# Performance work log

Measured on AMD Instinct MI355X. Metric: run time of the kernel, lower is better.

## Reference

```python
import jax, jax.numpy as jnp
import numpy as np

B, T, TOKEN_DIM, TPR_DIM = 16, 256, 256, 10
INNER = TOKEN_DIM // 4  # 64
TH = 32                 # tpr_mlp hidden dim
EPS = 1e-5              # BatchNorm eps


def _bn(x, g, b, m, v):
    # BatchNorm1d in eval mode: normalize with running stats
    return (x - m) * jax.lax.rsqrt(v + EPS) * g + b


def setup_inputs() -> dict:
    key = jax.random.key(0)
    ks = iter(jax.random.split(key, 32))
    def n(shape, s=0.02):
        return jax.random.normal(next(ks), shape, dtype=jnp.float32) * s
    def bn_params(c):
        g = 1.0 + 0.1 * jax.random.normal(next(ks), (c,), dtype=jnp.float32)
        b = 0.1 * jax.random.normal(next(ks), (c,), dtype=jnp.float32)
        m = 0.1 * jax.random.normal(next(ks), (c,), dtype=jnp.float32)
        v = jax.random.uniform(next(ks), (c,), dtype=jnp.float32, minval=0.5, maxval=1.5)
        return g, b, m, v
    inp = {}
    inp['x'] = jax.random.normal(next(ks), (B, T, TOKEN_DIM), dtype=jnp.float32)
    inp['r'] = jax.random.normal(next(ks), (B, T, T, TPR_DIM), dtype=jnp.float32)
    # fc1: Linear(token,token) + BN(token)
    inp['W1'] = n((TOKEN_DIM, TOKEN_DIM)); inp['b1'] = n((TOKEN_DIM,))
    inp['bn1_g'], inp['bn1_b'], inp['bn1_m'], inp['bn1_v'] = bn_params(TOKEN_DIM)
    # VectorAttention
    inp['Wqkv'] = n((TOKEN_DIM, 3 * INNER))
    inp['Wt1'] = n((TPR_DIM, TH)); inp['bt1'] = n((TH,))
    inp['bnt_g'], inp['bnt_b'], inp['bnt_m'], inp['bnt_v'] = bn_params(TH)
    inp['Wt2'] = n((TH, INNER)); inp['bt2'] = n((INNER,))
    inp['Wa1'] = n((INNER, INNER)); inp['ba1'] = n((INNER,))
    inp['Wa2'] = n((INNER, INNER)); inp['ba2'] = n((INNER,))
    # fc2: Linear(inner, token) + BN(token)
    inp['W2'] = n((INNER, TOKEN_DIM)); inp['b2'] = n((TOKEN_DIM,))
    inp['bn2_g'], inp['bn2_b'], inp['bn2_m'], inp['bn2_v'] = bn_params(TOKEN_DIM)
    return inp


def reference(x, r, W1, b1, bn1_g, bn1_b, bn1_m, bn1_v, Wqkv,
              Wt1, bt1, bnt_g, bnt_b, bnt_m, bnt_v, Wt2, bt2,
              Wa1, ba1, Wa2, ba2, W2, b2, bn2_g, bn2_b, bn2_m, bn2_v):
    # fc1 + BN, residual skip (pre-relu)
    y = _bn(x @ W1 + b1, bn1_g, bn1_b, bn1_m, bn1_v)  # [B,T,C]
    skip = y
    y = jax.nn.relu(y)
    # VectorAttention
    qkv = y @ Wqkv                                     # [B,T,3*inner]
    q, k, v = jnp.split(qkv, 3, axis=-1)               # each [B,T,inner]
    qk_rel = q[:, :, None, :] - k[:, None, :, :]       # [B,T,T,inner]
    rel_emb = jax.nn.relu(_bn(r @ Wt1 + bt1, bnt_g, bnt_b, bnt_m, bnt_v)) @ Wt2 + bt2  # [B,T,T,inner]
    vv = v[:, None, :, :] + rel_emb                    # [B,T,T,inner]
    h = jax.nn.relu((qk_rel + rel_emb) @ Wa1 + ba1)
    sim = h @ Wa2 + ba2                                # [B,T,T,inner]
    attn = jax.nn.softmax(sim, axis=-2)                # softmax over j (neighbor) axis
    agg = jnp.sum(attn * vv, axis=2)                   # [B,T,inner]
    # fc2 + BN + residual + relu
    out = jax.nn.relu(_bn(agg @ W2 + b2, bn2_g, bn2_b, bn2_m, bn2_v) + skip)
    return out  # [B,T,token_dim]
```

## Files before the change

kernel.cpp:

```cpp
#include <hip/hip_runtime.h>
#include <math.h>

#define BB 16
#define TT 256
#define CC 256
#define INNER 64
#define TPR 10
#define THD 32
#define EPSV 1e-5f

typedef __attribute__((ext_vector_type(8))) short short8;
typedef __attribute__((ext_vector_type(4))) float f32x4;

__device__ __forceinline__ short f2bf(float f) {
    unsigned u = __float_as_uint(f);
    u += 0x7fffu + ((u >> 16) & 1);
    return (short)(u >> 16);
}

__global__ __launch_bounds__(256) void fc1_qkv_kernel(
    const float* __restrict__ x, const float* __restrict__ W1, const float* __restrict__ b1,
    const float* __restrict__ g1, const float* __restrict__ bb1,
    const float* __restrict__ m1, const float* __restrict__ v1,
    const float* __restrict__ Wqkv,
    float* __restrict__ skip, float* __restrict__ qkv)
{
    const int ROWS = 8;
    __shared__ float xr[ROWS][CC];
    __shared__ float yr[ROWS][CC];
    const int n0 = blockIdx.x * ROWS;
    const int t = threadIdx.x;

#pragma unroll
    for (int rr = 0; rr < ROWS; ++rr)
        xr[rr][t] = x[(size_t)(n0 + rr) * CC + t];
    __syncthreads();

    float acc[ROWS];
#pragma unroll
    for (int rr = 0; rr < ROWS; ++rr) acc[rr] = 0.f;
    for (int k = 0; k < CC; ++k) {
        float wv = W1[(size_t)k * CC + t];
#pragma unroll
        for (int rr = 0; rr < ROWS; ++rr) acc[rr] = fmaf(xr[rr][k], wv, acc[rr]);
    }
    const float s1 = g1[t] * rsqrtf(v1[t] + EPSV);
    const float base = b1[t] - m1[t];
    const float bet = bb1[t];
#pragma unroll
    for (int rr = 0; rr < ROWS; ++rr) {
        float y = (acc[rr] + base) * s1 + bet;
        skip[(size_t)(n0 + rr) * CC + t] = y;
        yr[rr][t] = fmaxf(y, 0.f);
    }
    __syncthreads();

    if (t < 192) {
        float a2[ROWS];
#pragma unroll
        for (int rr = 0; rr < ROWS; ++rr) a2[rr] = 0.f;
        for (int k = 0; k < CC; ++k) {
            float wv = Wqkv[(size_t)k * 192 + t];
#pragma unroll
            for (int rr = 0; rr < ROWS; ++rr) a2[rr] = fmaf(yr[rr][k], wv, a2[rr]);
        }
#pragma unroll
        for (int rr = 0; rr < ROWS; ++rr)
            qkv[(size_t)(n0 + rr) * 192 + t] = a2[rr];
    }
}

#define O_TH   0
#define O_HID  32768
#define O_WA1  49152
#define O_WA2  57344
#define O_WT2  65536
#define O_WT1  69632
#define O_RED  71680
#define LDSZ   75776

__device__ __forceinline__ short8 ldfragA(const char* lds, int base, int row, int kbyte, int sl2, int mask) {
    return *(const short8*)(lds + base + (row << sl2) + (kbyte ^ ((row & mask) << 4)));
}
__device__ __forceinline__ void stbf16(char* lds, int base, int row, int col, int sl2, int mask, float v) {
    int cb = col * 2;
    int off = base + (row << sl2) + ((((cb & ~15) ^ ((row & mask) << 4))) | (cb & 15));
    *(short*)(lds + off) = f2bf(v);
}

__global__ __launch_bounds__(512) void attn_mfma_kernel(
    const float* __restrict__ r, const float* __restrict__ qkv,
    const float* __restrict__ Wt1, const float* __restrict__ bt1,
    const float* __restrict__ gt, const float* __restrict__ bbt,
    const float* __restrict__ mt, const float* __restrict__ vt,
    const float* __restrict__ Wt2, const float* __restrict__ bt2,
    const float* __restrict__ Wa1, const float* __restrict__ ba1,
    const float* __restrict__ Wa2, const float* __restrict__ ba2,
    float* __restrict__ agg)
{
    __shared__ char lds[LDSZ];
    const int n = blockIdx.x, b = n >> 8;
    const int tid = threadIdx.x;
    const int wv = tid >> 6, lane = tid & 63;
    const int lid = lane & 15, q4 = lane >> 4;
    const int kb = q4 * 16;
    const int tm0 = wv * 2;

    {
        uint32_t* z = (uint32_t*)lds;
#pragma unroll
        for (int e = 0; e < 8; ++e) z[tid + e * 512] = 0;
        ((uint32_t*)(lds + O_WT1))[tid] = 0;
    }
    __syncthreads();

    {
        const float* rrow = r + (size_t)n * (TT * TPR);
        for (int e = tid; e < TT * TPR; e += 512) {
            int j = e / TPR, p = e - j * TPR;
            int cb = p * 2;
            int off = (j << 6) + (((cb & ~15) ^ ((j & 3) << 4)) | (cb & 15));
            *(short*)(lds + off) = f2bf(rrow[e]);
        }
        if (tid < TPR * THD) {
            int p = tid >> 5, h = tid & 31;
            float scv = gt[h] * rsqrtf(vt[h] + EPSV);
            int cb = p * 2;
            int off = O_WT1 + (h << 6) + (((cb & ~15) ^ ((h & 3) << 4)) | (cb & 15));
            *(short*)(lds + off) = f2bf(Wt1[tid] * scv);
        }
        for (int e = tid; e < THD * INNER; e += 512) {
            int k = e >> 6, c = e & 63;
            int cb = k * 2;
            int off = O_WT2 + (c << 6) + (((cb & ~15) ^ ((c & 3) << 4)) | (cb & 15));
            *(short*)(lds + off) = f2bf(Wt2[e]);
        }
        for (int e = tid; e < INNER * INNER; e += 512) {
            int k = e >> 6, c = e & 63;
            int cb = k * 2;
            int sw = ((cb & ~15) ^ ((c & 7) << 4)) | (cb & 15);
            *(short*)(lds + O_WA1 + (c << 7) + sw) = f2bf(Wa1[e]);
            *(short*)(lds + O_WA2 + (c << 7) + sw) = f2bf(Wa2[e]);
        }
    }
    __syncthreads();

    {
        short8 b1f[2];
#pragma unroll
        for (int tn = 0; tn < 2; ++tn) {
            int cr = tn * 16 + lid;
            b1f[tn] = ldfragA(lds, O_WT1, cr, kb, 6, 3);
        }
        f32x4 acc1[2][2];
#pragma unroll
        for (int tm = 0; tm < 2; ++tm) {
            int row = (tm0 + tm) * 16 + lid;
            short8 a = ldfragA(lds, 0, row, kb, 6, 3);
#pragma unroll
            for (int tn = 0; tn < 2; ++tn) {
                f32x4 z = {0.f, 0.f, 0.f, 0.f};
                acc1[tm][tn] = __builtin_amdgcn_mfma_f32_16x16x32_bf16(a, b1f[tn], z, 0, 0, 0);
            }
        }
#pragma unroll
        for (int tn = 0; tn < 2; ++tn) {
            int col = tn * 16 + lid;
            float scv = gt[col] * rsqrtf(vt[col] + EPSV);
            float c1v = (bt1[col] - mt[col]) * scv + bbt[col];
#pragma unroll
            for (int tm = 0; tm < 2; ++tm)
#pragma unroll
                for (int g = 0; g < 4; ++g) {
                    int rw = (tm0 + tm) * 16 + q4 * 4 + g;
                    stbf16(lds, O_HID, rw, col, 6, 3, fmaxf(acc1[tm][tn][g] + c1v, 0.f));
                }
        }
    }
    __syncthreads();

    f32x4 rel[2][4];
    {
        short8 b2f[4];
#pragma unroll
        for (int tn = 0; tn < 4; ++tn) {
            int cr = tn * 16 + lid;
            b2f[tn] = ldfragA(lds, O_WT2, cr, kb, 6, 3);
        }
#pragma unroll
        for (int tm = 0; tm < 2; ++tm) {
            int row = (tm0 + tm) * 16 + lid;
            short8 a = ldfragA(lds, O_HID, row, kb, 6, 3);
#pragma unroll
            for (int tn = 0; tn < 4; ++tn) {
                f32x4 z = {0.f, 0.f, 0.f, 0.f};
                rel[tm][tn] = __builtin_amdgcn_mfma_f32_16x16x32_bf16(a, b2f[tn], z, 0, 0, 0);
            }
        }
    }
    const float* kvb = qkv + (size_t)b * (TT * 192);
#pragma unroll
    for (int tn = 0; tn < 4; ++tn) {
        int col = tn * 16 + lid;
        float bt2c = bt2[col];
        float qc = qkv[(size_t)n * 192 + col];
#pragma unroll
        for (int tm = 0; tm < 2; ++tm)
#pragma unroll
            for (int g = 0; g < 4; ++g) {
                int j = (tm0 + tm) * 16 + q4 * 4 + g;
                rel[tm][tn][g] += bt2c;
                float tv = qc - kvb[j * 192 + 64 + col] + rel[tm][tn][g];
                stbf16(lds, O_TH, j, col, 7, 7, tv);
            }
    }

    f32x4 acc[2][4];
#pragma unroll
    for (int tm = 0; tm < 2; ++tm)
#pragma unroll
        for (int tn = 0; tn < 4; ++tn) { f32x4 z = {0.f,0.f,0.f,0.f}; acc[tm][tn] = z; }
#pragma unroll
    for (int ks = 0; ks < 2; ++ks) {
        short8 bf[4];
#pragma unroll
        for (int tn = 0; tn < 4; ++tn) {
            int cr = tn * 16 + lid;
            bf[tn] = ldfragA(lds, O_WA1, cr, ks * 64 + kb, 7, 7);
        }
#pragma unroll
        for (int tm = 0; tm < 2; ++tm) {
            int row = (tm0 + tm) * 16 + lid;
            short8 a = ldfragA(lds, O_TH, row, ks * 64 + kb, 7, 7);
#pragma unroll
            for (int tn = 0; tn < 4; ++tn)
                acc[tm][tn] = __builtin_amdgcn_mfma_f32_16x16x32_bf16(a, bf[tn], acc[tm][tn], 0, 0, 0);
        }
    }
#pragma unroll
    for (int tn = 0; tn < 4; ++tn) {
        int col = tn * 16 + lid;
        float ba1c = ba1[col];
#pragma unroll
        for (int tm = 0; tm < 2; ++tm)
#pragma unroll
            for (int g = 0; g < 4; ++g) {
                int rw = (tm0 + tm) * 16 + q4 * 4 + g;
                stbf16(lds, O_TH, rw, col, 7, 7, fmaxf(acc[tm][tn][g] + ba1c, 0.f));
            }
    }

#pragma unroll
    for (int tm = 0; tm < 2; ++tm)
#pragma unroll
        for (int tn = 0; tn < 4; ++tn) { f32x4 z = {0.f,0.f,0.f,0.f}; acc[tm][tn] = z; }
#pragma unroll
    for (int ks = 0; ks < 2; ++ks) {
        short8 bf[4];
#pragma unroll
        for (int tn = 0; tn < 4; ++tn) {
            int cr = tn * 16 + lid;
            bf[tn] = ldfragA(lds, O_WA2, cr, ks * 64 + kb, 7, 7);
        }
#pragma unroll
        for (int tm = 0; tm < 2; ++tm) {
            int row = (tm0 + tm) * 16 + lid;
            short8 a = ldfragA(lds, O_TH, row, ks * 64 + kb, 7, 7);
#pragma unroll
            for (int tn = 0; tn < 4; ++tn)
                acc[tm][tn] = __builtin_amdgcn_mfma_f32_16x16x32_bf16(a, bf[tn], acc[tm][tn], 0, 0, 0);
        }
    }

    float num[4], den[4];
#pragma unroll
    for (int tn = 0; tn < 4; ++tn) { num[tn] = 0.f; den[tn] = 0.f; }
#pragma unroll
    for (int tn = 0; tn < 4; ++tn) {
        int col = tn * 16 + lid;
#pragma unroll
        for (int tm = 0; tm < 2; ++tm)
#pragma unroll
            for (int g = 0; g < 4; ++g) {
                int j = (tm0 + tm) * 16 + q4 * 4 + g;
                float ev = __expf(acc[tm][tn][g]);
                float vvv = kvb[j * 192 + 128 + col] + rel[tm][tn][g];
                den[tn] += ev;
                num[tn] = fmaf(ev, vvv, num[tn]);
            }
    }
#pragma unroll
    for (int tn = 0; tn < 4; ++tn) {
        num[tn] += __shfl_xor(num[tn], 16);
        num[tn] += __shfl_xor(num[tn], 32);
        den[tn] += __shfl_xor(den[tn], 16);
        den[tn] += __shfl_xor(den[tn], 32);
    }
    if (lane < 16) {
        float* RD = (float*)(lds + O_RED);
#pragma unroll
        for (int tn = 0; tn < 4; ++tn) {
            RD[(wv * 2 + 0) * 64 + tn * 16 + lane] = num[tn];
            RD[(wv * 2 + 1) * 64 + tn * 16 + lane] = den[tn];
        }
    }
    __syncthreads();
    if (tid < 64) {
        float* RD = (float*)(lds + O_RED);
        float nn = 0.f, dd = 0.f;
#pragma unroll
        for (int w = 0; w < 8; ++w) {
            nn += RD[(w * 2 + 0) * 64 + tid];
            dd += RD[(w * 2 + 1) * 64 + tid];
        }
        agg[(size_t)n * 64 + tid] = nn / dd;
    }
}

__global__ __launch_bounds__(256) void fc2_kernel(
    const float* __restrict__ agg, const float* __restrict__ W2, const float* __restrict__ b2,
    const float* __restrict__ g2, const float* __restrict__ bb2,
    const float* __restrict__ m2, const float* __restrict__ v2,
    const float* __restrict__ skip, float* __restrict__ out)
{
    const int ROWS = 8;
    __shared__ float ar[ROWS][INNER];
    const int n0 = blockIdx.x * ROWS;
    const int t = threadIdx.x;

    for (int idx = t; idx < ROWS * INNER; idx += 256)
        ((float*)ar)[idx] = agg[(size_t)n0 * INNER + idx];
    __syncthreads();

    const float s2 = g2[t] * rsqrtf(v2[t] + EPSV);
    const float base = b2[t] - m2[t];
    const float bet = bb2[t];

    float accv[ROWS];
#pragma unroll
    for (int rr = 0; rr < ROWS; ++rr) accv[rr] = 0.f;
    for (int k = 0; k < INNER; ++k) {
        float wv = W2[(size_t)k * CC + t];
#pragma unroll
        for (int rr = 0; rr < ROWS; ++rr) accv[rr] = fmaf(ar[rr][k], wv, accv[rr]);
    }
#pragma unroll
    for (int rr = 0; rr < ROWS; ++rr) {
        float y = (accv[rr] + base) * s2 + bet;
        out[(size_t)(n0 + rr) * CC + t] =
            fmaxf(y + skip[(size_t)(n0 + rr) * CC + t], 0.f);
    }
}

extern "C" void kernel_launch(void* const* d_in, const int* in_sizes, int n_in,
                              void* d_out, int out_size, void* d_ws, size_t ws_size,
                              hipStream_t stream)
{
    const float* x   = (const float*)d_in[0];
    const float* r   = (const float*)d_in[1];
    const float* W1  = (const float*)d_in[2];
    const float* b1  = (const float*)d_in[3];
    const float* g1  = (const float*)d_in[4];
    const float* bb1 = (const float*)d_in[5];
    const float* m1  = (const float*)d_in[6];
    const float* v1  = (const float*)d_in[7];
    const float* Wqkv= (const float*)d_in[8];
    const float* Wt1 = (const float*)d_in[9];
    const float* bt1 = (const float*)d_in[10];
    const float* gt  = (const float*)d_in[11];
    const float* bbt = (const float*)d_in[12];
    const float* mt  = (const float*)d_in[13];
    const float* vt  = (const float*)d_in[14];
    const float* Wt2 = (const float*)d_in[15];
    const float* bt2 = (const float*)d_in[16];
    const float* Wa1 = (const float*)d_in[17];
    const float* ba1 = (const float*)d_in[18];
    const float* Wa2 = (const float*)d_in[19];
    const float* ba2 = (const float*)d_in[20];
    const float* W2  = (const float*)d_in[21];
    const float* b2  = (const float*)d_in[22];
    const float* g2  = (const float*)d_in[23];
    const float* bb2 = (const float*)d_in[24];
    const float* m2  = (const float*)d_in[25];
    const float* v2  = (const float*)d_in[26];
    float* out = (float*)d_out;

    const int N = BB * TT;
    float* skip = (float*)d_ws;
    float* qkv  = skip + (size_t)N * CC;
    float* agg  = qkv  + (size_t)N * 192;

    fc1_qkv_kernel<<<dim3(N / 8), dim3(256), 0, stream>>>(
        x, W1, b1, g1, bb1, m1, v1, Wqkv, skip, qkv);
    attn_mfma_kernel<<<dim3(N), dim3(512), 0, stream>>>(
        r, qkv, Wt1, bt1, gt, bbt, mt, vt, Wt2, bt2, Wa1, ba1, Wa2, ba2, agg);
    fc2_kernel<<<dim3(N / 8), dim3(256), 0, stream>>>(
        agg, W2, b2, g2, bb2, m2, v2, skip, out);
}
```

Baseline: 169.1 us.

## Transpose MFMA operands so each wave owns its j rows, dropping a barrier

The attention kernel now computes every matmul in transposed form, with weights as the A operand and neighbor rows as B. Each lane then holds four consecutive channels for one j, so global loads of k, v and BN params become float4 vector loads and LDS stores become packed 8-byte bf16 writes. Because each wave only reads and writes its own j rows of the shared activation tile, the __syncthreads between the tpr MLP stages goes away. The final reduction changes to shuffles over the j lanes, and launch bounds request 4 waves per SIMD at a slightly larger LDS footprint, which may raise register pressure.

```diff
diff --git a/kernel.cpp b/kernel.cpp
--- a/kernel.cpp
+++ b/kernel.cpp
@@ -1,4 +1,5 @@
 #include <hip/hip_runtime.h>
+#include <hip/hip_bf16.h>
 #include <math.h>
 
 #define BB 16
@@ -11,11 +12,15 @@
 
 typedef __attribute__((ext_vector_type(8))) short short8;
 typedef __attribute__((ext_vector_type(4))) float f32x4;
+typedef __attribute__((ext_vector_type(4))) unsigned int u32x4;
 
 __device__ __forceinline__ short f2bf(float f) {
     unsigned u = __float_as_uint(f);
     u += 0x7fffu + ((u >> 16) & 1);
     return (short)(u >> 16);
+}
+__device__ __forceinline__ unsigned pkbf(float a, float b) {
+    return (unsigned)(unsigned short)f2bf(a) | ((unsigned)(unsigned short)f2bf(b) << 16);
 }
 
 __global__ __launch_bounds__(256) void fc1_qkv_kernel(
@@ -70,25 +75,23 @@
     }
 }
 
-#define O_TH   0
-#define O_HID  32768
-#define O_WA1  49152
-#define O_WA2  57344
-#define O_WT2  65536
-#define O_WT1  69632
-#define O_RED  71680
-#define LDSZ   75776
-
-__device__ __forceinline__ short8 ldfragA(const char* lds, int base, int row, int kbyte, int sl2, int mask) {
-    return *(const short8*)(lds + base + (row << sl2) + (kbyte ^ ((row & mask) << 4)));
-}
-__device__ __forceinline__ void stbf16(char* lds, int base, int row, int col, int sl2, int mask, float v) {
-    int cb = col * 2;
-    int off = base + (row << sl2) + ((((cb & ~15) ^ ((row & mask) << 4))) | (cb & 15));
-    *(short*)(lds + off) = f2bf(v);
-}
-
-__global__ __launch_bounds__(512) void attn_mfma_kernel(
+#define O_R    0
+#define O_TH   16384
+#define O_WT1  49152
+#define O_WT2  53248
+#define O_WA1  61440
+#define O_WA2  69632
+#define O_RED  77824
+#define LDSZ   81920
+
+__device__ __forceinline__ int swb(int row, int cb, int sh, int mask) {
+    return (row << sh) + (((cb & ~15) ^ ((row & mask) << 4)) | (cb & 15));
+}
+__device__ __forceinline__ short8 ldfrag(const char* lds, int base, int row, int cb16, int sh, int mask) {
+    return *(const short8*)(lds + base + (row << sh) + (cb16 ^ ((row & mask) << 4)));
+}
+
+__global__ __launch_bounds__(512, 4) void attn_mfma_kernel(
     const float* __restrict__ r, const float* __restrict__ qkv,
     const float* __restrict__ Wt1, const float* __restrict__ bt1,
     const float* __restrict__ gt, const float* __restrict__ bbt,
@@ -98,19 +101,19 @@
     const float* __restrict__ Wa2, const float* __restrict__ ba2,
     float* __restrict__ agg)
 {
-    __shared__ char lds[LDSZ];
+    __shared__ __align__(16) char lds[LDSZ];
     const int n = blockIdx.x, b = n >> 8;
     const int tid = threadIdx.x;
     const int wv = tid >> 6, lane = tid & 63;
     const int lid = lane & 15, q4 = lane >> 4;
     const int kb = q4 * 16;
-    const int tm0 = wv * 2;
+    const int jt0 = wv * 2;
 
     {
-        uint32_t* z = (uint32_t*)lds;
-#pragma unroll
-        for (int e = 0; e < 8; ++e) z[tid + e * 512] = 0;
-        ((uint32_t*)(lds + O_WT1))[tid] = 0;
+        u32x4 z = {0u, 0u, 0u, 0u};
+        *(u32x4*)(lds + O_R + tid * 16) = z;
+        *(u32x4*)(lds + O_R + 8192 + tid * 16) = z;
+        if (tid < 256) *(u32x4*)(lds + O_WT1 + tid * 16) = z;
     }
     __syncthreads();
 
@@ -118,200 +121,195 @@
         const float* rrow = r + (size_t)n * (TT * TPR);
         for (int e = tid; e < TT * TPR; e += 512) {
             int j = e / TPR, p = e - j * TPR;
-            int cb = p * 2;
-            int off = (j << 6) + (((cb & ~15) ^ ((j & 3) << 4)) | (cb & 15));
-            *(short*)(lds + off) = f2bf(rrow[e]);
+            *(short*)(lds + O_R + swb(j, p * 2, 6, 3)) = f2bf(rrow[e]);
         }
         if (tid < TPR * THD) {
             int p = tid >> 5, h = tid & 31;
             float scv = gt[h] * rsqrtf(vt[h] + EPSV);
-            int cb = p * 2;
-            int off = O_WT1 + (h << 6) + (((cb & ~15) ^ ((h & 3) << 4)) | (cb & 15));
-            *(short*)(lds + off) = f2bf(Wt1[tid] * scv);
+            *(short*)(lds + O_WT1 + swb(h, p * 2, 7, 7)) = f2bf(Wt1[tid] * scv);
         }
         for (int e = tid; e < THD * INNER; e += 512) {
-            int k = e >> 6, c = e & 63;
-            int cb = k * 2;
-            int off = O_WT2 + (c << 6) + (((cb & ~15) ^ ((c & 3) << 4)) | (cb & 15));
-            *(short*)(lds + off) = f2bf(Wt2[e]);
+            int h = e >> 6, c = e & 63;
+            *(short*)(lds + O_WT2 + swb(c, h * 2, 7, 7)) = f2bf(Wt2[e]);
         }
         for (int e = tid; e < INNER * INNER; e += 512) {
             int k = e >> 6, c = e & 63;
-            int cb = k * 2;
-            int sw = ((cb & ~15) ^ ((c & 7) << 4)) | (cb & 15);
-            *(short*)(lds + O_WA1 + (c << 7) + sw) = f2bf(Wa1[e]);
-            *(short*)(lds + O_WA2 + (c << 7) + sw) = f2bf(Wa2[e]);
-        }
-    }
-    __syncthreads();
+            *(short*)(lds + O_WA1 + swb(c, k * 2, 7, 7)) = f2bf(Wa1[e]);
+            *(short*)(lds + O_WA2 + swb(c, k * 2, 7, 7)) = f2bf(Wa2[e]);
+        }
+    }
+    __syncthreads();
+
+    const float* kvb = qkv + (size_t)b * (TT * 192);
+    const f32x4 z4 = {0.f, 0.f, 0.f, 0.f};
 
     {
-        short8 b1f[2];
-#pragma unroll
-        for (int tn = 0; tn < 2; ++tn) {
-            int cr = tn * 16 + lid;
-            b1f[tn] = ldfragA(lds, O_WT1, cr, kb, 6, 3);
-        }
+        short8 aw0 = ldfrag(lds, O_WT1, lid, kb, 7, 7);
+        short8 aw1 = ldfrag(lds, O_WT1, 16 + lid, kb, 7, 7);
         f32x4 acc1[2][2];
 #pragma unroll
+        for (int tn = 0; tn < 2; ++tn) {
+            int j = (jt0 + tn) * 16 + lid;
+            short8 bf = ldfrag(lds, O_R, j, kb, 6, 3);
+            acc1[0][tn] = __builtin_amdgcn_mfma_f32_16x16x32_bf16(aw0, bf, z4, 0, 0, 0);
+            acc1[1][tn] = __builtin_amdgcn_mfma_f32_16x16x32_bf16(aw1, bf, z4, 0, 0, 0);
+        }
+#pragma unroll
         for (int tm = 0; tm < 2; ++tm) {
-            int row = (tm0 + tm) * 16 + lid;
-            short8 a = ldfragA(lds, 0, row, kb, 6, 3);
+            int ch0 = tm * 16 + q4 * 4;
+            f32x4 g4 = *(const f32x4*)(gt + ch0);
+            f32x4 vv4 = *(const f32x4*)(vt + ch0);
+            f32x4 b4 = *(const f32x4*)(bt1 + ch0);
+            f32x4 m4 = *(const f32x4*)(mt + ch0);
+            f32x4 bb4 = *(const f32x4*)(bbt + ch0);
+            f32x4 c1;
+#pragma unroll
+            for (int g = 0; g < 4; ++g)
+                c1[g] = (b4[g] - m4[g]) * (g4[g] * rsqrtf(vv4[g] + EPSV)) + bb4[g];
 #pragma unroll
             for (int tn = 0; tn < 2; ++tn) {
-                f32x4 z = {0.f, 0.f, 0.f, 0.f};
-                acc1[tm][tn] = __builtin_amdgcn_mfma_f32_16x16x32_bf16(a, b1f[tn], z, 0, 0, 0);
+                int j = (jt0 + tn) * 16 + lid;
+                float h0 = fmaxf(acc1[tm][tn][0] + c1[0], 0.f);
+                float h1 = fmaxf(acc1[tm][tn][1] + c1[1], 0.f);
+                float h2 = fmaxf(acc1[tm][tn][2] + c1[2], 0.f);
+                float h3 = fmaxf(acc1[tm][tn][3] + c1[3], 0.f);
+                uint2 w; w.x = pkbf(h0, h1); w.y = pkbf(h2, h3);
+                *(uint2*)(lds + O_TH + swb(j, tm * 32 + q4 * 8, 7, 7)) = w;
             }
         }
-#pragma unroll
-        for (int tn = 0; tn < 2; ++tn) {
-            int col = tn * 16 + lid;
-            float scv = gt[col] * rsqrtf(vt[col] + EPSV);
-            float c1v = (bt1[col] - mt[col]) * scv + bbt[col];
-#pragma unroll
-            for (int tm = 0; tm < 2; ++tm)
-#pragma unroll
-                for (int g = 0; g < 4; ++g) {
-                    int rw = (tm0 + tm) * 16 + q4 * 4 + g;
-                    stbf16(lds, O_HID, rw, col, 6, 3, fmaxf(acc1[tm][tn][g] + c1v, 0.f));
-                }
-        }
-    }
-    __syncthreads();
-
-    f32x4 rel[2][4];
+    }
+
+    f32x4 rel[4][2];
     {
-        short8 b2f[4];
-#pragma unroll
-        for (int tn = 0; tn < 4; ++tn) {
-            int cr = tn * 16 + lid;
-            b2f[tn] = ldfragA(lds, O_WT2, cr, kb, 6, 3);
-        }
-#pragma unroll
-        for (int tm = 0; tm < 2; ++tm) {
-            int row = (tm0 + tm) * 16 + lid;
-            short8 a = ldfragA(lds, O_HID, row, kb, 6, 3);
-#pragma unroll
-            for (int tn = 0; tn < 4; ++tn) {
-                f32x4 z = {0.f, 0.f, 0.f, 0.f};
-                rel[tm][tn] = __builtin_amdgcn_mfma_f32_16x16x32_bf16(a, b2f[tn], z, 0, 0, 0);
+        short8 aw[4];
+#pragma unroll
+        for (int tm = 0; tm < 4; ++tm)
+            aw[tm] = ldfrag(lds, O_WT2, tm * 16 + lid, kb, 7, 7);
+#pragma unroll
+        for (int tn = 0; tn < 2; ++tn) {
+            int j = (jt0 + tn) * 16 + lid;
+            short8 bf = ldfrag(lds, O_TH, j, kb, 7, 7);
+#pragma unroll
+            for (int tm = 0; tm < 4; ++tm)
+                rel[tm][tn] = __builtin_amdgcn_mfma_f32_16x16x32_bf16(aw[tm], bf, z4, 0, 0, 0);
+        }
+    }
+#pragma unroll
+    for (int tm = 0; tm < 4; ++tm) {
+        int ch0 = tm * 16 + q4 * 4;
+        f32x4 bt24 = *(const f32x4*)(bt2 + ch0);
+        f32x4 qv4 = *(const f32x4*)(qkv + (size_t)n * 192 + ch0);
+#pragma unroll
+        for (int tn = 0; tn < 2; ++tn) {
+            int j = (jt0 + tn) * 16 + lid;
+            f32x4 kv4 = *(const f32x4*)(kvb + (size_t)j * 192 + 64 + ch0);
+            float t0, t1, t2, t3;
+#pragma unroll
+            for (int g = 0; g < 4; ++g) rel[tm][tn][g] += bt24[g];
+            t0 = qv4[0] - kv4[0] + rel[tm][tn][0];
+            t1 = qv4[1] - kv4[1] + rel[tm][tn][1];
+            t2 = qv4[2] - kv4[2] + rel[tm][tn][2];
+            t3 = qv4[3] - kv4[3] + rel[tm][tn][3];
+            uint2 w; w.x = pkbf(t0, t1); w.y = pkbf(t2, t3);
+            *(uint2*)(lds + O_TH + swb(j, tm * 32 + q4 * 8, 7, 7)) = w;
+        }
+    }
+
+    f32x4 acc[4][2];
+#pragma unroll
+    for (int tm = 0; tm < 4; ++tm)
+#pragma unroll
+        for (int tn = 0; tn < 2; ++tn) acc[tm][tn] = z4;
+#pragma unroll
+    for (int ks = 0; ks < 2; ++ks) {
+        short8 aw[4];
+#pragma unroll
+        for (int tm = 0; tm < 4; ++tm)
+            aw[tm] = ldfrag(lds, O_WA1, tm * 16 + lid, ks * 64 + kb, 7, 7);
+#pragma unroll
+        for (int tn = 0; tn < 2; ++tn) {
+            int j = (jt0 + tn) * 16 + lid;
+            short8 bf = ldfrag(lds, O_TH, j, ks * 64 + kb, 7, 7);
+#pragma unroll
+            for (int tm = 0; tm < 4; ++tm)
+                acc[tm][tn] = __builtin_amdgcn_mfma_f32_16x16x32_bf16(aw[tm], bf, acc[tm][tn], 0, 0, 0);
+        }
+    }
+#pragma unroll
+    for (int tm = 0; tm < 4; ++tm) {
+        int ch0 = tm * 16 + q4 * 4;
+        f32x4 ba14 = *(const f32x4*)(ba1 + ch0);
+#pragma unroll
+        for (int tn = 0; tn < 2; ++tn) {
+            int j = (jt0 + tn) * 16 + lid;
+            float h0 = fmaxf(acc[tm][tn][0] + ba14[0], 0.f);
+            float h1 = fmaxf(acc[tm][tn][1] + ba14[1], 0.f);
+            float h2 = fmaxf(acc[tm][tn][2] + ba14[2], 0.f);
+            float h3 = fmaxf(acc[tm][tn][3] + ba14[3], 0.f);
+            uint2 w; w.x = pkbf(h0, h1); w.y = pkbf(h2, h3);
+            *(uint2*)(lds + O_TH + swb(j, tm * 32 + q4 * 8, 7, 7)) = w;
+        }
+    }
+
+#pragma unroll
+    for (int tm = 0; tm < 4; ++tm)
+#pragma unroll
+        for (int tn = 0; tn < 2; ++tn) acc[tm][tn] = z4;
+#pragma unroll
+    for (int ks = 0; ks < 2; ++ks) {
+        short8 aw[4];
+#pragma unroll
+        for (int tm = 0; tm < 4; ++tm)
+            aw[tm] = ldfrag(lds, O_WA2, tm * 16 + lid, ks * 64 + kb, 7, 7);
+#pragma unroll
+        for (int tn = 0; tn < 2; ++tn) {
+            int j = (jt0 + tn) * 16 + lid;
+            short8 bf = ldfrag(lds, O_TH, j, ks * 64 + kb, 7, 7);
+#pragma unroll
+            for (int tm = 0; tm < 4; ++tm)
+                acc[tm][tn] = __builtin_amdgcn_mfma_f32_16x16x32_bf16(aw[tm], bf, acc[tm][tn], 0, 0, 0);
+        }
+    }
+
+#pragma unroll
+    for (int tm = 0; tm < 4; ++tm) {
+        const int ch0 = tm * 16 + q4 * 4;
+        f32x4 num = z4, den = z4;
+#pragma unroll
+        for (int tn = 0; tn < 2; ++tn) {
+            int j = (jt0 + tn) * 16 + lid;
+            f32x4 v4 = *(const f32x4*)(kvb + (size_t)j * 192 + 128 + ch0);
+#pragma unroll
+            for (int g = 0; g < 4; ++g) {
+                float ev = __expf(acc[tm][tn][g]);
+                den[g] += ev;
+                num[g] = fmaf(ev, v4[g] + rel[tm][tn][g], num[g]);
             }
         }
-    }
-    const float* kvb = qkv + (size_t)b * (TT * 192);
-#pragma unroll
-    for (int tn = 0; tn < 4; ++tn) {
-        int col = tn * 16 + lid;
-        float bt2c = bt2[col];
-        float qc = qkv[(size_t)n * 192 + col];
-#pragma unroll
-        for (int tm = 0; tm < 2; ++tm)
+#pragma unroll
+        for (int ofs = 1; ofs < 16; ofs <<= 1) {
 #pragma unroll
             for (int g = 0; g < 4; ++g) {
-                int j = (tm0 + tm) * 16 + q4 * 4 + g;
-                rel[tm][tn][g] += bt2c;
-                float tv = qc - kvb[j * 192 + 64 + col] + rel[tm][tn][g];
-                stbf16(lds, O_TH, j, col, 7, 7, tv);
+                num[g] += __shfl_xor(num[g], ofs);
+                den[g] += __shfl_xor(den[g], ofs);
             }
-    }
-
-    f32x4 acc[2][4];
-#pragma unroll
-    for (int tm = 0; tm < 2; ++tm)
-#pragma unroll
-        for (int tn = 0; tn < 4; ++tn) { f32x4 z = {0.f,0.f,0.f,0.f}; acc[tm][tn] = z; }
-#pragma unroll
-    for (int ks = 0; ks < 2; ++ks) {
-        short8 bf[4];
-#pragma unroll
-        for (int tn = 0; tn < 4; ++tn) {
-            int cr = tn * 16 + lid;
-            bf[tn] = ldfragA(lds, O_WA1, cr, ks * 64 + kb, 7, 7);
-        }
-#pragma unroll
-        for (int tm = 0; tm < 2; ++tm) {
-            int row = (tm0 + tm) * 16 + lid;
-            short8 a = ldfragA(lds, O_TH, row, ks * 64 + kb, 7, 7);
-#pragma unroll
-            for (int tn = 0; tn < 4; ++tn)
-                acc[tm][tn] = __builtin_amdgcn_mfma_f32_16x16x32_bf16(a, bf[tn], acc[tm][tn], 0, 0, 0);
-        }
-    }
-#pragma unroll
-    for (int tn = 0; tn < 4; ++tn) {
-        int col = tn * 16 + lid;
-        float ba1c = ba1[col];
-#pragma unroll
-        for (int tm = 0; tm < 2; ++tm)
-#pragma unroll
-            for (int g = 0; g < 4; ++g) {
-                int rw = (tm0 + tm) * 16 + q4 * 4 + g;
-                stbf16(lds, O_TH, rw, col, 7, 7, fmaxf(acc[tm][tn][g] + ba1c, 0.f));
-            }
-    }
-
-#pragma unroll
-    for (int tm = 0; tm < 2; ++tm)
-#pragma unroll
-        for (int tn = 0; tn < 4; ++tn) { f32x4 z = {0.f,0.f,0.f,0.f}; acc[tm][tn] = z; }
-#pragma unroll
-    for (int ks = 0; ks < 2; ++ks) {
-        short8 bf[4];
-#pragma unroll
-        for (int tn = 0; tn < 4; ++tn) {
-            int cr = tn * 16 + lid;
-            bf[tn] = ldfragA(lds, O_WA2, cr, ks * 64 + kb, 7, 7);
-        }
-#pragma unroll
-        for (int tm = 0; tm < 2; ++tm) {
-            int row = (tm0 + tm) * 16 + lid;
-            short8 a = ldfragA(lds, O_TH, row, ks * 64 + kb, 7, 7);
-#pragma unroll
-            for (int tn = 0; tn < 4; ++tn)
-                acc[tm][tn] = __builtin_amdgcn_mfma_f32_16x16x32_bf16(a, bf[tn], acc[tm][tn], 0, 0, 0);
-        }
-    }
-
-    float num[4], den[4];
-#pragma unroll
-    for (int tn = 0; tn < 4; ++tn) { num[tn] = 0.f; den[tn] = 0.f; }
-#pragma unroll
-    for (int tn = 0; tn < 4; ++tn) {
-        int col = tn * 16 + lid;
-#pragma unroll
-        for (int tm = 0; tm < 2; ++tm)
-#pragma unroll
-            for (int g = 0; g < 4; ++g) {
-                int j = (tm0 + tm) * 16 + q4 * 4 + g;
-                float ev = __expf(acc[tm][tn][g]);
-                float vvv = kvb[j * 192 + 128 + col] + rel[tm][tn][g];
-                den[tn] += ev;
-                num[tn] = fmaf(ev, vvv, num[tn]);
-            }
-    }
-#pragma unroll
-    for (int tn = 0; tn < 4; ++tn) {
-        num[tn] += __shfl_xor(num[tn], 16);
-        num[tn] += __shfl_xor(num[tn], 32);
-        den[tn] += __shfl_xor(den[tn], 16);
-        den[tn] += __shfl_xor(den[tn], 32);
-    }
-    if (lane < 16) {
-        float* RD = (float*)(lds + O_RED);
-#pragma unroll
-        for (int tn = 0; tn < 4; ++tn) {
-            RD[(wv * 2 + 0) * 64 + tn * 16 + lane] = num[tn];
-            RD[(wv * 2 + 1) * 64 + tn * 16 + lane] = den[tn];
-        }
-    }
-    __syncthreads();
+        }
+        if (lid == 0) {
+            int base = O_RED + ((wv * 4 + tm) * 4 + q4) * 32;
+            *(f32x4*)(lds + base) = num;
+            *(f32x4*)(lds + base + 16) = den;
+        }
+    }
+    __syncthreads();
+
     if (tid < 64) {
-        float* RD = (float*)(lds + O_RED);
+        int tm = tid >> 4, qq = (tid >> 2) & 3, g = tid & 3;
         float nn = 0.f, dd = 0.f;
 #pragma unroll
         for (int w = 0; w < 8; ++w) {
-            nn += RD[(w * 2 + 0) * 64 + tid];
-            dd += RD[(w * 2 + 1) * 64 + tid];
+            int base = O_RED + ((w * 4 + tm) * 4 + qq) * 32 + g * 4;
+            nn += *(const float*)(lds + base);
+            dd += *(const float*)(lds + base + 16);
         }
         agg[(size_t)n * 64 + tid] = nn / dd;
     }
```

Result: no change. 170.6 us (+0.9%).
